# Kernel optimization log

Hardware: AMD Instinct MI355X
Metric: run time of the kernel (lower is better)

Reference implementation:

```python
import jax, jax.numpy as jnp
import numpy as np

B, S, D = 1, 2048, 2048
NH, NKV, HD = 16, 8, 128
FF = 8192
L = 2
V = 32000
THETA = 10000.0
EPS = 1e-5
SCALE = 0.02


def setup_inputs() -> dict:
    key = jax.random.key(0)
    ks = jax.random.split(key, 16)
    return {
        "input_ids": jax.random.randint(ks[0], (B, S), 0, V, dtype=jnp.int32),
        "embed": jax.random.normal(ks[1], (V, D), jnp.float32) * SCALE,
        "Wq": jax.random.normal(ks[2], (L, D, NH * HD), jnp.float32) * SCALE,
        "Wk": jax.random.normal(ks[3], (L, D, NKV * HD), jnp.float32) * SCALE,
        "Wv": jax.random.normal(ks[4], (L, D, NKV * HD), jnp.float32) * SCALE,
        "Wo": jax.random.normal(ks[5], (L, NH * HD, D), jnp.float32) * SCALE,
        "Wgate": jax.random.normal(ks[6], (L, D, FF), jnp.float32) * SCALE,
        "Wup": jax.random.normal(ks[7], (L, D, FF), jnp.float32) * SCALE,
        "Wdown": jax.random.normal(ks[8], (L, FF, D), jnp.float32) * SCALE,
        "norm_attn": jnp.ones((L, D), jnp.float32),
        "norm_mlp": jnp.ones((L, D), jnp.float32),
        "norm_final": jnp.ones((D,), jnp.float32),
        "lm_head": jax.random.normal(ks[9], (D, V), jnp.float32) * SCALE,
        "D1": jax.random.normal(ks[10], (S,), jnp.float32) + 2.0,
        "D2": jax.random.normal(ks[11], (HD,), jnp.float32) + 2.0,
        "D3": jax.random.normal(ks[12], (S,), jnp.float32) + 2.0,
    }


def _rms_norm(x, w):
    return x * jax.lax.rsqrt(jnp.mean(x * x, axis=-1, keepdims=True) + EPS) * w


def _rotate_half(x):
    x1, x2 = jnp.split(x, 2, axis=-1)
    return jnp.concatenate([-x2, x1], axis=-1)


def _forward(input_ids, embed, Wq, Wk, Wv, Wo, Wgate, Wup, Wdown,
             norm_attn, norm_mlp, norm_final, lm_head, D1, D2, D3):
    # RoPE tables: [1,1,S,HD]
    inv_freq = 1.0 / (THETA ** (jnp.arange(0, HD, 2, dtype=jnp.float32) / HD))
    freqs = jnp.arange(S, dtype=jnp.float32)[:, None] * inv_freq[None, :]
    emb = jnp.concatenate([freqs, freqs], axis=-1)
    cos = jnp.cos(emb)[None, None]
    sin = jnp.sin(emb)[None, None]
    causal = jnp.tril(jnp.ones((S, S), dtype=bool))
    neg = jnp.finfo(jnp.float32).min
    D1i, D2i, D3i = 1.0 / D1, 1.0 / D2, 1.0 / D3
    n_rep = NH // NKV

    h = embed[input_ids]  # [B,S,D]
    for l in range(L):
        # --- attention block ---
        x = _rms_norm(h, norm_attn[l])
        q = (x @ Wq[l]).reshape(B, S, NH, HD).transpose(0, 2, 1, 3)   # [B,NH,S,HD]
        k = (x @ Wk[l]).reshape(B, S, NKV, HD).transpose(0, 2, 1, 3)  # [B,NKV,S,HD]
        v = (x @ Wv[l]).reshape(B, S, NKV, HD).transpose(0, 2, 1, 3)
        q = q * cos + _rotate_half(q) * sin
        k = k * cos + _rotate_half(k) * sin
        # repeat_kv (GQA)
        k = jnp.repeat(k, n_rep, axis=1)
        v = jnp.repeat(v, n_rep, axis=1)
        # TEE diagonal encryption: Q' = D1 Q D2, K'^T = D2^-1 K^T D3
        q_enc = q * D1[None, None, :, None] * D2[None, None, None, :]
        k_enc = k * D3[None, None, :, None] * D2i[None, None, None, :]
        scores = jnp.einsum('bhqd,bhkd->bhqk', q_enc, k_enc)
        # decrypt: D1^-1 (Q'K'^T) D3^-1  (mathematically cancels encryption)
        scores = scores * D1i[None, None, :, None] * D3i[None, None, None, :]
        scores = scores / jnp.sqrt(jnp.float32(HD))
        scores = jnp.where(causal[None, None], scores, neg)
        probs = jax.nn.softmax(scores, axis=-1)
        o = jnp.einsum('bhqk,bhkd->bhqd', probs, v)
        o = o.transpose(0, 2, 1, 3).reshape(B, S, NH * HD)
        h = h + o @ Wo[l]
        # --- SwiGLU MLP block ---
        x = _rms_norm(h, norm_mlp[l])
        h = h + (jax.nn.silu(x @ Wgate[l]) * (x @ Wup[l])) @ Wdown[l]

    h = _rms_norm(h, norm_final)
    return h @ lm_head  # logits [B,S,V]


def reference(input_ids, embed, Wq, Wk, Wv, Wo, Wgate, Wup, Wdown,
              norm_attn, norm_mlp, norm_final, lm_head, D1, D2, D3):
    return _forward(input_ids, embed, Wq, Wk, Wv, Wo, Wgate, Wup, Wdown,
                    norm_attn, norm_mlp, norm_final, lm_head, D1, D2, D3)
```

## Files before the change

### kernel.cpp

```cpp
#include <hip/hip_runtime.h>
#include <cstdint>
#include <cstddef>

typedef __attribute__((ext_vector_type(4))) float f32x4;
typedef __attribute__((ext_vector_type(8))) short short8;
typedef __attribute__((ext_vector_type(4))) unsigned int u32x4;

static const int TS = 2048;
static const int DM = 2048;
static const int NHEAD = 16, NKVH = 8, HDIM = 128;
static const int FFD = 8192;
static const int NVOC = 32000;
static const int QKVN = 4096;

__device__ __forceinline__ unsigned short f2bf(float f){
  unsigned int u = __builtin_bit_cast(unsigned int, f);
  u += 0x7FFFu + ((u >> 16) & 1u);
  return (unsigned short)(u >> 16);
}
__device__ __forceinline__ float bf2f(short h){
  unsigned int u = ((unsigned int)(unsigned short)h) << 16;
  return __builtin_bit_cast(float, u);
}
__device__ __forceinline__ f32x4 mfma16(short8 a, short8 b, f32x4 c){
  return __builtin_amdgcn_mfma_f32_16x16x32_bf16(a, b, c, 0, 0, 0);
}
__device__ __forceinline__ void gload16(const void* g, void* l){
  __builtin_amdgcn_global_load_lds(
      (const __attribute__((address_space(1))) unsigned int*)g,
      (__attribute__((address_space(3))) unsigned int*)l, 16, 0, 0);
}
__device__ __forceinline__ long toff(int r, int k, int ldk){
  return ((long)((r >> 4) * ldk + (k >> 5)) << 9)
       + (((k & 31) >> 3) << 7) + ((r & 15) << 3) + (k & 7);
}

__global__ void rope_tables_k(float* __restrict__ cosT, float* __restrict__ sinT){
  int idx = blockIdx.x * 256 + threadIdx.x;
  int s = idx >> 6, j = idx & 63;
  float inv = exp2f(-(float)j * (13.287712379549449f / 64.0f));
  float ang = (float)s * inv;
  cosT[idx] = cosf(ang);
  sinT[idx] = sinf(ang);
}

__global__ void embed_k(const int* __restrict__ ids, const float* __restrict__ E,
                        float* __restrict__ h){
  int s = blockIdx.x, tid = threadIdx.x;
  long id = ids[s];
  const f32x4* src = (const f32x4*)(E + id * (long)DM);
  f32x4* dst = (f32x4*)(h + (long)s * DM);
  dst[tid] = src[tid];
  dst[tid + 256] = src[tid + 256];
}

__global__ void rmsnorm_k(const float* __restrict__ x, const float* __restrict__ w,
                          short* __restrict__ out){
  int s = blockIdx.x, tid = threadIdx.x;
  const float* row = x + (long)s * DM;
  f32x4 v0 = *(const f32x4*)&row[tid * 8];
  f32x4 v1 = *(const f32x4*)&row[tid * 8 + 4];
  float ss = v0[0]*v0[0] + v0[1]*v0[1] + v0[2]*v0[2] + v0[3]*v0[3]
           + v1[0]*v1[0] + v1[1]*v1[1] + v1[2]*v1[2] + v1[3]*v1[3];
  #pragma unroll
  for (int off = 32; off; off >>= 1) ss += __shfl_xor(ss, off);
  __shared__ float sred[4];
  int wave = tid >> 6, lane = tid & 63;
  if (lane == 0) sred[wave] = ss;
  __syncthreads();
  float tot = sred[0] + sred[1] + sred[2] + sred[3];
  float r = rsqrtf(tot * (1.0f / (float)DM) + 1e-5f);
  f32x4 w0 = *(const f32x4*)&w[tid * 8];
  f32x4 w1 = *(const f32x4*)&w[tid * 8 + 4];
  short8 o;
  #pragma unroll
  for (int j = 0; j < 4; j++) o[j] = (short)f2bf(v0[j] * r * w0[j]);
  #pragma unroll
  for (int j = 0; j < 4; j++) o[4 + j] = (short)f2bf(v1[j] * r * w1[j]);
  *(short8*)&out[toff(s, tid * 8, DM >> 5)] = o;
}

__global__ void transpose_k(const float* __restrict__ B, short* __restrict__ Bt,
                            int K, int N){
  __shared__ float t[64][65];
  int tid = threadIdx.x;
  int kb = blockIdx.y * 64, nb = blockIdx.x * 64;
  int r0 = tid >> 4, c4 = tid & 15;
  const int ldk = K >> 5;
  #pragma unroll
  for (int p = 0; p < 4; p++){
    int r = r0 + p * 16;
    f32x4 v = *(const f32x4*)&B[(long)(kb + r) * N + nb + c4 * 4];
    t[r][c4*4+0] = v[0]; t[r][c4*4+1] = v[1]; t[r][c4*4+2] = v[2]; t[r][c4*4+3] = v[3];
  }
  __syncthreads();
  int n0 = tid >> 3, k0 = (tid & 7) * 8;
  #pragma unroll
  for (int p = 0; p < 2; p++){
    int n = n0 + p * 32;
    short8 o;
    #pragma unroll
    for (int j = 0; j < 8; j++) o[j] = (short)f2bf(t[k0 + j][n]);
    *(short8*)&Bt[toff(nb + n, kb + k0, ldk)] = o;
  }
}

__global__ void vtrans_k(const short* __restrict__ vb, short* __restrict__ vtb, int stride){
  int s0 = blockIdx.x * 64, kv = blockIdx.y;
  int tid = threadIdx.x;
  int s = s0 + (tid & 63);
  int d0 = (tid >> 6) * 8;
  #pragma unroll
  for (int p = 0; p < 4; p++){
    int d = d0 + p * 32;
    short8 v = *(const short8*)&vb[(long)s * stride + kv * HDIM + d];
    #pragma unroll
    for (int j = 0; j < 8; j++)
      vtb[(long)(kv * HDIM + d + j) * TS + s] = v[j];
  }
}

__global__ void rope_apply_k(short* __restrict__ buf, const float* __restrict__ cosT,
                             const float* __restrict__ sinT, int nh, int stride, int coloff){
  int idx = blockIdx.x * 256 + threadIdx.x;
  int j = idx & 63;
  int t = idx >> 6;
  int hh = t % nh;
  int s = t / nh;
  long base = (long)s * stride + coloff + hh * HDIM + j;
  float c = cosT[s * 64 + j], sn = sinT[s * 64 + j];
  float x1 = bf2f(buf[base]), x2 = bf2f(buf[base + 64]);
  buf[base]      = (short)f2bf(x1 * c - x2 * sn);
  buf[base + 64] = (short)f2bf(x2 * c + x1 * sn);
}

__global__ void reduce4_k(const float* __restrict__ p, float* __restrict__ h){
  const long stride = (long)TS * DM;
  long i = ((long)blockIdx.x * 256 + threadIdx.x) * 4;
  f32x4 a = *(const f32x4*)&h[i];
  f32x4 v0 = *(const f32x4*)&p[i];
  f32x4 v1 = *(const f32x4*)&p[i + stride];
  f32x4 v2 = *(const f32x4*)&p[i + 2 * stride];
  f32x4 v3 = *(const f32x4*)&p[i + 3 * stride];
  a = a + ((v0 + v1) + (v2 + v3));
  *(f32x4*)&h[i] = a;
}

template<int EPI>
__global__ __launch_bounds__(512, 2)
void gemm256(const short* __restrict__ A, int ldkA,
             const short* __restrict__ Bt, int ldkB,
             float* __restrict__ Cf, short* __restrict__ Cb,
             const short* __restrict__ Xtra, int N, int K, int ldkC){
  __shared__ short lds[4][2][8192];
  const int tid = threadIdx.x;
  const int wid = tid >> 6, lane = tid & 63;
  const int wr = wid >> 2, wc = wid & 3;
  const int fr = lane & 15, fch = lane >> 4;
  const int nt = K >> 5;

  const int z = blockIdx.y;
  const int k0 = z * nt;

  const int nbt = N >> 8;
  const int nwg = nbt << 3;
  const int q = nwg >> 3;
  const int swz = (blockIdx.x & 7) * q + (blockIdx.x >> 3);
  const int mb = swz & 7, nb = swz >> 3;

  const short* Abase = A  + ((long)(mb * 16) * ldkA + k0) * 512 + lane * 8;
  const short* Bbase = Bt + ((long)(nb * 16) * ldkB + k0) * 512 + lane * 8;
  const int gA0 = wid * 2, gA1 = wid * 2 + 1;

  short8 aE[4], aO[4], bE[2], bO[2];
  f32x4 acc[8][4] = {};

#define STG_A(bufc, g_, tau_) \
  gload16(Abase + ((long)(g_) * ldkA + (tau_)) * 512, &lds[bufc][0][(g_) * 512])
#define STG_B(bufc, g_, tau_) \
  gload16(Bbase + ((long)(g_) * ldkB + (tau_)) * 512, &lds[bufc][1][(g_) * 512])
#define RDA(dst, bufc, mh) do{ \
    _Pragma("unroll") \
    for (int j_ = 0; j_ < 4; j_++) \
      dst[j_] = *(const short8*)&lds[bufc][0][(wr * 8 + (mh) * 4 + j_) * 512 + fch * 128 + fr * 8]; \
  }while(0)
#define RDB(dst, bufc, nh) do{ \
    _Pragma("unroll") \
    for (int i_ = 0; i_ < 2; i_++) \
      dst[i_] = *(const short8*)&lds[bufc][1][(wc * 4 + (nh) * 2 + i_) * 512 + fch * 128 + fr * 8]; \
  }while(0)
#define MM8(va, vb, mh, nh) do{ \
    __builtin_amdgcn_s_setprio(1); \
    _Pragma("unroll") \
    for (int j_ = 0; j_ < 4; j_++) \
      _Pragma("unroll") \
      for (int i_ = 0; i_ < 2; i_++) \
        acc[(mh)*4+j_][(nh)*2+i_] = mfma16(va[j_], vb[i_], acc[(mh)*4+j_][(nh)*2+i_]); \
    __builtin_amdgcn_s_setprio(0); \
  }while(0)
#define SB __builtin_amdgcn_sched_barrier(0)

#define TILE(t_, bufR, bufN, bufS, bC, bNx) do{ \
    const int tau_ = ((t_) + 2 < nt) ? (t_) + 2 : nt - 1; \
    RDB(bNx, bufR, 1); STG_A(bufS, gA0, tau_); SB; MM8(aE, bC, 0, 0); \
    RDA(aO,  bufR, 1); STG_A(bufS, gA1, tau_); SB; MM8(aE, bNx, 0, 1); \
    asm volatile("s_waitcnt vmcnt(2)" ::: "memory"); \
    __builtin_amdgcn_s_barrier(); \
    RDA(aE,  bufN, 0); STG_B(bufS, gA0, tau_); SB; MM8(aO, bNx, 1, 1); \
    RDB(bNx, bufN, 0); STG_B(bufS, gA1, tau_); SB; MM8(aO, bC, 1, 0); \
    __builtin_amdgcn_s_barrier(); \
  }while(0)

  STG_A(0, gA0, 0); STG_A(0, gA1, 0); STG_B(0, gA0, 0); STG_B(0, gA1, 0);
  STG_A(1, gA0, 1); STG_A(1, gA1, 1); STG_B(1, gA0, 1); STG_B(1, gA1, 1);
  asm volatile("s_waitcnt vmcnt(4)" ::: "memory");
  __builtin_amdgcn_s_barrier();
  RDA(aE, 0, 0); RDB(bE, 0, 0);

  const int nIter = nt >> 2;
  for (int it = 0; it < nIter; ++it){
    const int t0 = it << 2;
    TILE(t0 + 0, 0, 1, 2, bE, bO);
    TILE(t0 + 1, 1, 2, 3, bO, bE);
    TILE(t0 + 2, 2, 3, 0, bE, bO);
    TILE(t0 + 3, 3, 0, 1, bO, bE);
  }

#undef STG_A
#undef STG_B
#undef RDA
#undef RDB
#undef MM8
#undef SB
#undef TILE

  const int rb0 = mb * 256 + wr * 128 + fch * 4;
  const int cb0 = nb * 256 + wc * 64 + fr;
  const long pbase = (EPI == 5) ? (long)z * ((long)TS * N) : 0;
  #pragma unroll
  for (int m = 0; m < 8; m++)
    #pragma unroll
    for (int n = 0; n < 4; n++)
      #pragma unroll
      for (int i = 0; i < 4; i++){
        const int rr = rb0 + m * 16 + i, cc = cb0 + n * 16;
        long idx = (long)rr * N + cc;
        float v = acc[m][n][i];
        if constexpr (EPI == 0) Cf[idx] = v;
        else if constexpr (EPI == 1) Cb[idx] = (short)f2bf(v);
        else if constexpr (EPI == 3){
          float sg = 1.0f / (1.0f + __expf(-v));
          Cb[idx] = (short)f2bf(v * sg);
        } else if constexpr (EPI == 4){
          float g = bf2f(Xtra[idx]);
          Cb[toff(rr, cc, ldkC)] = (short)f2bf(g * v);
        } else {
          Cf[pbase + idx] = v;
        }
      }
}

template<int EPI>
__global__ __launch_bounds__(256)
void gemm_bt(const short* __restrict__ A, int ldkA,
             const short* __restrict__ Bt, int ldkB,
             float* __restrict__ Cf, short* __restrict__ Cb,
             const short* __restrict__ Xtra, int N, int K){
  __shared__ short As[4096];
  __shared__ short Bs[4096];
  const int tid = threadIdx.x;
  const int wave = tid >> 6, lane = tid & 63;
  const int wr = wave >> 1, wc = wave & 1;
  const int mb = blockIdx.y, nb = blockIdx.x;

  const short* Abase = A  + (long)(mb * 8) * ldkA * 512 + lane * 8;
  const short* Bbase = Bt + (long)(nb * 8) * ldkB * 512 + lane * 8;

  f32x4 acc[4][4] = {};
  const int fr = lane & 15, fch = lane >> 4;
  const int nt = K >> 5;

  for (int tau = 0; tau < nt; tau++){
    __syncthreads();
    gload16(Abase + ((long)wave * ldkA + tau) * 512,       &As[wave * 512]);
    gload16(Abase + ((long)(wave + 4) * ldkA + tau) * 512, &As[(4 + wave) * 512]);
    gload16(Bbase + ((long)wave * ldkB + tau) * 512,       &Bs[wave * 512]);
    gload16(Bbase + ((long)(wave + 4) * ldkB + tau) * 512, &Bs[(4 + wave) * 512]);
    __syncthreads();
    short8 a[4], b[4];
    #pragma unroll
    for (int m = 0; m < 4; m++)
      a[m] = *(const short8*)&As[(wr * 4 + m) * 512 + fch * 128 + fr * 8];
    #pragma unroll
    for (int n = 0; n < 4; n++)
      b[n] = *(const short8*)&Bs[(wc * 4 + n) * 512 + fch * 128 + fr * 8];
    #pragma unroll
    for (int m = 0; m < 4; m++)
      #pragma unroll
      for (int n = 0; n < 4; n++)
        acc[m][n] = mfma16(a[m], b[n], acc[m][n]);
  }

  const int rb = mb * 128 + wr * 64 + (lane >> 4) * 4;
  const int cb = nb * 128 + wc * 64 + (lane & 15);
  #pragma unroll
  for (int m = 0; m < 4; m++)
    #pragma unroll
    for (int n = 0; n < 4; n++)
      #pragma unroll
      for (int i = 0; i < 4; i++){
        long idx = (long)(rb + m * 16 + i) * N + (cb + n * 16);
        float v = acc[m][n][i];
        if constexpr (EPI == 0) Cf[idx] = v;
        else if constexpr (EPI == 1) Cb[idx] = (short)f2bf(v);
        else if constexpr (EPI == 2) Cf[idx] += v;
        else if constexpr (EPI == 3){
          float sg = 1.0f / (1.0f + __expf(-v));
          Cb[idx] = (short)f2bf(v * sg);
        } else {
          float g = bf2f(Xtra[idx]);
          Cb[idx] = (short)f2bf(g * v);
        }
      }
}

__device__ __forceinline__ int qoff(int r, int cB){ return r * 256 + (cB ^ ((r & 7) << 4)); }
__device__ __forceinline__ int voff(int d, int cB){ return d * 128 + (cB ^ ((d & 7) << 4)); }
__device__ __forceinline__ int poff(int r, int cB){ return r * 128 + (cB ^ ((r & 7) << 4)); }

__global__ __launch_bounds__(256)
void attn_k(const short* __restrict__ qb, const short* __restrict__ kb,
            const short* __restrict__ vtb, short* __restrict__ ob){
  __shared__ short Qs[64 * 128];
  __shared__ short Ks[64 * 128];
  __shared__ short Vt[128 * 64];
  __shared__ short Ps[64 * 64];
  const int tid = threadIdx.x, wave = tid >> 6, lane = tid & 63;
  const int qt = blockIdx.x, head = blockIdx.y, kvh = head >> 1;
  const float scale = 0.08838834764831845f;

  {
    int r0 = tid >> 4, c16 = tid & 15;
    #pragma unroll
    for (int p = 0; p < 4; p++){
      int r = r0 + p * 16;
      u32x4 v = *(const u32x4*)&qb[(long)(qt * 64 + r) * QKVN + head * HDIM + c16 * 8];
      *(u32x4*)((char*)Qs + qoff(r, c16 * 16)) = v;
    }
  }

  float mrun[4] = {-1e30f, -1e30f, -1e30f, -1e30f};
  float lrun[4] = {0.f, 0.f, 0.f, 0.f};
  f32x4 accO[8] = {};

  for (int kt = 0; kt <= qt; kt++){
    __syncthreads();
    {
      int r0 = tid >> 4, c16 = tid & 15;
      #pragma unroll
      for (int p = 0; p < 4; p++){
        int r = r0 + p * 16;
        u32x4 v = *(const u32x4*)&kb[(long)(kt * 64 + r) * QKVN + kvh * HDIM + c16 * 8];
        *(u32x4*)((char*)Ks + qoff(r, c16 * 16)) = v;
      }
      int vr0 = tid >> 3, vc = tid & 7;
      #pragma unroll
      for (int p = 0; p < 4; p++){
        int d = vr0 + p * 32;
        u32x4 v = *(const u32x4*)&vtb[(long)(kvh * HDIM + d) * TS + kt * 64 + vc * 8];
        *(u32x4*)((char*)Vt + voff(d, vc * 16)) = v;
      }
    }
    __syncthreads();

    f32x4 sacc[4] = {};
    #pragma unroll
    for (int k4 = 0; k4 < 4; k4++){
      short8 aq = *(const short8*)((const char*)Qs +
                   qoff(wave * 16 + (lane & 15), k4 * 64 + (lane >> 4) * 16));
      #pragma unroll
      for (int n = 0; n < 4; n++){
        short8 bk = *(const short8*)((const char*)Ks +
                     qoff(n * 16 + (lane & 15), k4 * 64 + (lane >> 4) * 16));
        sacc[n] = mfma16(aq, bk, sacc[n]);
      }
    }

    const bool diag = (kt == qt);
    float mt[4] = {-1e30f, -1e30f, -1e30f, -1e30f};
    #pragma unroll
    for (int n = 0; n < 4; n++)
      #pragma unroll
      for (int i = 0; i < 4; i++){
        float v = sacc[n][i] * scale;
        if (diag){
          int rr = (lane >> 4) * 4 + i + wave * 16;
          int cc = n * 16 + (lane & 15);
          if (cc > rr) v = -1e30f;
        }
        sacc[n][i] = v;
        mt[i] = fmaxf(mt[i], v);
      }
    #pragma unroll
    for (int off = 1; off < 16; off <<= 1)
      #pragma unroll
      for (int i = 0; i < 4; i++) mt[i] = fmaxf(mt[i], __shfl_xor(mt[i], off));
    float alpha[4], rsum[4];
    #pragma unroll
    for (int i = 0; i < 4; i++){
      float mn = fmaxf(mrun[i], mt[i]);
      alpha[i] = __expf(mrun[i] - mn);
      mrun[i] = mn;
      rsum[i] = 0.f;
    }
    #pragma unroll
    for (int n = 0; n < 4; n++)
      #pragma unroll
      for (int i = 0; i < 4; i++){
        float p = __expf(sacc[n][i] - mrun[i]);
        sacc[n][i] = p;
        rsum[i] += p;
      }
    #pragma unroll
    for (int off = 1; off < 16; off <<= 1)
      #pragma unroll
      for (int i = 0; i < 4; i++) rsum[i] += __shfl_xor(rsum[i], off);
    #pragma unroll
    for (int i = 0; i < 4; i++) lrun[i] = lrun[i] * alpha[i] + rsum[i];

    #pragma unroll
    for (int n = 0; n < 4; n++)
      #pragma unroll
      for (int i = 0; i < 4; i++){
        int rr = wave * 16 + (lane >> 4) * 4 + i;
        int cc = n * 16 + (lane & 15);
        *(short*)((char*)Ps + poff(rr, cc * 2)) = (short)f2bf(sacc[n][i]);
      }

    #pragma unroll
    for (int n = 0; n < 8; n++)
      #pragma unroll
      for (int i = 0; i < 4; i++) accO[n][i] *= alpha[i];
    #pragma unroll
    for (int ks = 0; ks < 2; ks++){
      short8 ap = *(const short8*)((const char*)Ps +
                   poff(wave * 16 + (lane & 15), ks * 64 + (lane >> 4) * 16));
      #pragma unroll
      for (int n = 0; n < 8; n++){
        short8 bv = *(const short8*)((const char*)Vt +
                     voff(n * 16 + (lane & 15), ks * 64 + (lane >> 4) * 16));
        accO[n] = mfma16(ap, bv, accO[n]);
      }
    }
  }

  #pragma unroll
  for (int i = 0; i < 4; i++){
    float inv = 1.0f / lrun[i];
    int rr = qt * 64 + wave * 16 + (lane >> 4) * 4 + i;
    #pragma unroll
    for (int n = 0; n < 8; n++){
      int cc = head * HDIM + n * 16 + (lane & 15);
      ob[toff(rr, cc, DM >> 5)] = (short)f2bf(accO[n][i] * inv);
    }
  }
}

extern "C" void kernel_launch(void* const* d_in, const int* in_sizes, int n_in,
                              void* d_out, int out_size, void* d_ws, size_t ws_size,
                              hipStream_t stream){
  (void)in_sizes; (void)n_in; (void)out_size; (void)ws_size;
  const int*   ids = (const int*)d_in[0];
  const float* E   = (const float*)d_in[1];
  const float* Wq  = (const float*)d_in[2];
  const float* Wk  = (const float*)d_in[3];
  const float* Wv  = (const float*)d_in[4];
  const float* Wo  = (const float*)d_in[5];
  const float* Wg  = (const float*)d_in[6];
  const float* Wu  = (const float*)d_in[7];
  const float* Wd  = (const float*)d_in[8];
  const float* nA  = (const float*)d_in[9];
  const float* nM  = (const float*)d_in[10];
  const float* nF  = (const float*)d_in[11];
  const float* LMH = (const float*)d_in[12];
  float* out = (float*)d_out;

  char* ws = (char*)d_ws;
  size_t off = 0;
  auto alloc = [&](size_t bytes){ void* p = ws + off; off += (bytes + 255) & ~(size_t)255; return p; };
  float* h    = (float*)alloc((size_t)TS * DM * 4);
  short* xb   = (short*)alloc((size_t)TS * DM * 2);
  short* qkvb = (short*)alloc((size_t)TS * QKVN * 2);
  short* vtb  = (short*)alloc((size_t)NKVH * HDIM * TS * 2);
  short* obuf = (short*)alloc((size_t)TS * DM * 2);
  short* sg   = (short*)alloc((size_t)TS * FFD * 2);
  short* actb = (short*)alloc((size_t)TS * FFD * 2);
  float* cosT = (float*)alloc((size_t)TS * 64 * 4);
  float* sinT = (float*)alloc((size_t)TS * 64 * 4);
  short* wT   = (short*)alloc((size_t)NVOC * DM * 2);
  float* pPart = (float*)((char*)wT + (size_t)36 * 1024 * 1024);

  rope_tables_k<<<512, 256, 0, stream>>>(cosT, sinT);
  embed_k<<<TS, 256, 0, stream>>>(ids, E, h);

  for (int l = 0; l < 2; l++){
    rmsnorm_k<<<TS, 256, 0, stream>>>(h, nA + (size_t)l * DM, xb);
    transpose_k<<<dim3(32, 32), 256, 0, stream>>>(Wq + (size_t)l * DM * DM, wT, DM, DM);
    transpose_k<<<dim3(16, 32), 256, 0, stream>>>(Wk + (size_t)l * DM * 1024, wT + (size_t)2048 * DM, DM, 1024);
    transpose_k<<<dim3(16, 32), 256, 0, stream>>>(Wv + (size_t)l * DM * 1024, wT + (size_t)3072 * DM, DM, 1024);
    gemm256<1><<<dim3(128), 512, 0, stream>>>(xb, 64, wT, 64, nullptr, qkvb, nullptr, QKVN, DM, 0);
    rope_apply_k<<<8192, 256, 0, stream>>>(qkvb, cosT, sinT, NHEAD, QKVN, 0);
    rope_apply_k<<<4096, 256, 0, stream>>>(qkvb, cosT, sinT, NKVH, QKVN, 2048);
    vtrans_k<<<dim3(32, 8), 256, 0, stream>>>(qkvb + 3072, vtb, QKVN);
    attn_k<<<dim3(32, 16), 256, 0, stream>>>(qkvb, qkvb + 2048, vtb, obuf);
    transpose_k<<<dim3(32, 32), 256, 0, stream>>>(Wo + (size_t)l * DM * DM, wT, DM, DM);
    gemm_bt<2><<<dim3(16, 16), 256, 0, stream>>>(obuf, 64, wT, 64, h, nullptr, nullptr, DM, DM);
    rmsnorm_k<<<TS, 256, 0, stream>>>(h, nM + (size_t)l * DM, xb);
    transpose_k<<<dim3(128, 32), 256, 0, stream>>>(Wg + (size_t)l * DM * FFD, wT, DM, FFD);
    gemm256<3><<<dim3(256), 512, 0, stream>>>(xb, 64, wT, 64, nullptr, sg, nullptr, FFD, DM, 0);
    transpose_k<<<dim3(128, 32), 256, 0, stream>>>(Wu + (size_t)l * DM * FFD, wT, DM, FFD);
    gemm256<4><<<dim3(256), 512, 0, stream>>>(xb, 64, wT, 64, nullptr, actb, sg, FFD, DM, FFD >> 5);
    transpose_k<<<dim3(32, 128), 256, 0, stream>>>(Wd + (size_t)l * FFD * DM, wT, FFD, DM);
    gemm256<5><<<dim3(64, 4), 512, 0, stream>>>(actb, 256, wT, 256, pPart, nullptr, nullptr, DM, FFD / 4, 0);
    reduce4_k<<<4096, 256, 0, stream>>>(pPart, h);
  }

  rmsnorm_k<<<TS, 256, 0, stream>>>(h, nF, xb);
  transpose_k<<<dim3(500, 32), 256, 0, stream>>>(LMH, wT, DM, NVOC);
  gemm256<0><<<dim3(1000), 512, 0, stream>>>(xb, 64, wT, 64, out, nullptr, nullptr, NVOC, DM, 0);
}
```

Before: 1.403 ms.

## Deepen gemm256 prefetch to three stages and route Wo projection through split-K gemm256

The 4-buffer LDS pipeline in gemm256 now prefetches three tiles ahead instead of two, with adjusted vmcnt waits, a three-stage prologue, and a final drain. The Wo output projection, previously done by a simple single-buffered 128x128 gemm_bt with in-place accumulate, now uses the pipelined 256x256 gemm256 with a 4-way split-K into partial buffers followed by reduce4_k into h. This is meant to hide more global-load latency and use the faster GEMM path for Wo. The cost is an extra reduction kernel and partial-buffer traffic, plus more in-flight loads per wave.

```diff
diff --git a/kernel.cpp b/kernel.cpp
--- a/kernel.cpp
+++ b/kernel.cpp
@@ -201,10 +201,10 @@
 #define SB __builtin_amdgcn_sched_barrier(0)
 
 #define TILE(t_, bufR, bufN, bufS, bC, bNx) do{ \
-    const int tau_ = ((t_) + 2 < nt) ? (t_) + 2 : nt - 1; \
+    const int tau_ = ((t_) + 3 < nt) ? (t_) + 3 : nt - 1; \
     RDB(bNx, bufR, 1); STG_A(bufS, gA0, tau_); SB; MM8(aE, bC, 0, 0); \
     RDA(aO,  bufR, 1); STG_A(bufS, gA1, tau_); SB; MM8(aE, bNx, 0, 1); \
-    asm volatile("s_waitcnt vmcnt(2)" ::: "memory"); \
+    asm volatile("s_waitcnt vmcnt(6)" ::: "memory"); \
     __builtin_amdgcn_s_barrier(); \
     RDA(aE,  bufN, 0); STG_B(bufS, gA0, tau_); SB; MM8(aO, bNx, 1, 1); \
     RDB(bNx, bufN, 0); STG_B(bufS, gA1, tau_); SB; MM8(aO, bC, 1, 0); \
@@ -213,18 +213,20 @@
 
   STG_A(0, gA0, 0); STG_A(0, gA1, 0); STG_B(0, gA0, 0); STG_B(0, gA1, 0);
   STG_A(1, gA0, 1); STG_A(1, gA1, 1); STG_B(1, gA0, 1); STG_B(1, gA1, 1);
-  asm volatile("s_waitcnt vmcnt(4)" ::: "memory");
+  STG_A(2, gA0, 2); STG_A(2, gA1, 2); STG_B(2, gA0, 2); STG_B(2, gA1, 2);
+  asm volatile("s_waitcnt vmcnt(8)" ::: "memory");
   __builtin_amdgcn_s_barrier();
   RDA(aE, 0, 0); RDB(bE, 0, 0);
 
   const int nIter = nt >> 2;
   for (int it = 0; it < nIter; ++it){
     const int t0 = it << 2;
-    TILE(t0 + 0, 0, 1, 2, bE, bO);
-    TILE(t0 + 1, 1, 2, 3, bO, bE);
-    TILE(t0 + 2, 2, 3, 0, bE, bO);
-    TILE(t0 + 3, 3, 0, 1, bO, bE);
-  }
+    TILE(t0 + 0, 0, 1, 3, bE, bO);
+    TILE(t0 + 1, 1, 2, 0, bO, bE);
+    TILE(t0 + 2, 2, 3, 1, bE, bO);
+    TILE(t0 + 3, 3, 0, 2, bO, bE);
+  }
+  asm volatile("s_waitcnt vmcnt(0)" ::: "memory");
 
 #undef STG_A
 #undef STG_B
@@ -256,70 +258,6 @@
           Cb[toff(rr, cc, ldkC)] = (short)f2bf(g * v);
         } else {
           Cf[pbase + idx] = v;
-        }
-      }
-}
-
-template<int EPI>
-__global__ __launch_bounds__(256)
-void gemm_bt(const short* __restrict__ A, int ldkA,
-             const short* __restrict__ Bt, int ldkB,
-             float* __restrict__ Cf, short* __restrict__ Cb,
-             const short* __restrict__ Xtra, int N, int K){
-  __shared__ short As[4096];
-  __shared__ short Bs[4096];
-  const int tid = threadIdx.x;
-  const int wave = tid >> 6, lane = tid & 63;
-  const int wr = wave >> 1, wc = wave & 1;
-  const int mb = blockIdx.y, nb = blockIdx.x;
-
-  const short* Abase = A  + (long)(mb * 8) * ldkA * 512 + lane * 8;
-  const short* Bbase = Bt + (long)(nb * 8) * ldkB * 512 + lane * 8;
-
-  f32x4 acc[4][4] = {};
-  const int fr = lane & 15, fch = lane >> 4;
-  const int nt = K >> 5;
-
-  for (int tau = 0; tau < nt; tau++){
-    __syncthreads();
-    gload16(Abase + ((long)wave * ldkA + tau) * 512,       &As[wave * 512]);
-    gload16(Abase + ((long)(wave + 4) * ldkA + tau) * 512, &As[(4 + wave) * 512]);
-    gload16(Bbase + ((long)wave * ldkB + tau) * 512,       &Bs[wave * 512]);
-    gload16(Bbase + ((long)(wave + 4) * ldkB + tau) * 512, &Bs[(4 + wave) * 512]);
-    __syncthreads();
-    short8 a[4], b[4];
-    #pragma unroll
-    for (int m = 0; m < 4; m++)
-      a[m] = *(const short8*)&As[(wr * 4 + m) * 512 + fch * 128 + fr * 8];
-    #pragma unroll
-    for (int n = 0; n < 4; n++)
-      b[n] = *(const short8*)&Bs[(wc * 4 + n) * 512 + fch * 128 + fr * 8];
-    #pragma unroll
-    for (int m = 0; m < 4; m++)
-      #pragma unroll
-      for (int n = 0; n < 4; n++)
-        acc[m][n] = mfma16(a[m], b[n], acc[m][n]);
-  }
-
-  const int rb = mb * 128 + wr * 64 + (lane >> 4) * 4;
-  const int cb = nb * 128 + wc * 64 + (lane & 15);
-  #pragma unroll
-  for (int m = 0; m < 4; m++)
-    #pragma unroll
-    for (int n = 0; n < 4; n++)
-      #pragma unroll
-      for (int i = 0; i < 4; i++){
-        long idx = (long)(rb + m * 16 + i) * N + (cb + n * 16);
-        float v = acc[m][n][i];
-        if constexpr (EPI == 0) Cf[idx] = v;
-        else if constexpr (EPI == 1) Cb[idx] = (short)f2bf(v);
-        else if constexpr (EPI == 2) Cf[idx] += v;
-        else if constexpr (EPI == 3){
-          float sg = 1.0f / (1.0f + __expf(-v));
-          Cb[idx] = (short)f2bf(v * sg);
-        } else {
-          float g = bf2f(Xtra[idx]);
-          Cb[idx] = (short)f2bf(g * v);
         }
       }
 }
@@ -514,7 +452,8 @@
     vtrans_k<<<dim3(32, 8), 256, 0, stream>>>(qkvb + 3072, vtb, QKVN);
     attn_k<<<dim3(32, 16), 256, 0, stream>>>(qkvb, qkvb + 2048, vtb, obuf);
     transpose_k<<<dim3(32, 32), 256, 0, stream>>>(Wo + (size_t)l * DM * DM, wT, DM, DM);
-    gemm_bt<2><<<dim3(16, 16), 256, 0, stream>>>(obuf, 64, wT, 64, h, nullptr, nullptr, DM, DM);
+    gemm256<5><<<dim3(64, 4), 512, 0, stream>>>(obuf, 64, wT, 64, pPart, nullptr, nullptr, DM, DM / 4, 0);
+    reduce4_k<<<4096, 256, 0, stream>>>(pPart, h);
     rmsnorm_k<<<TS, 256, 0, stream>>>(h, nM + (size_t)l * DM, xb);
     transpose_k<<<dim3(128, 32), 256, 0, stream>>>(Wg + (size_t)l * DM * FFD, wT, DM, FFD);
     gemm256<3><<<dim3(256), 512, 0, stream>>>(xb, 64, wT, 64, nullptr, sg, nullptr, FFD, DM, 0);
```

Measured after the change: 1.359 ms. 1.03x faster.
